# Performance work log

Hardware: AMD Instinct MI355X
Metric: run time of the kernel (lower is better)

Reference implementation:

```python
import jax, jax.numpy as jnp
import numpy as np

MAX_SPAN_WIDTH = 32  # static bound on (end - start) + 1 span length


def setup_inputs() -> dict:
    key = jax.random.key(0)
    k1, k2, k3, k4 = jax.random.split(key, 4)
    B, T, D, N = 4, 2048, 768, 512
    sequence_tensor = jax.random.normal(k1, (B, T, D), dtype=jnp.float32)
    starts = jax.random.randint(k2, (B, N), 0, T - MAX_SPAN_WIDTH)
    widths = jax.random.randint(k3, (B, N), 0, MAX_SPAN_WIDTH)
    span_indices = jnp.stack([starts, starts + widths], axis=-1)  # inclusive ends
    att_w = jax.random.normal(k4, (D, 1), dtype=jnp.float32) * 0.02
    att_b = jnp.zeros((1,), dtype=jnp.float32)
    return {"sequence_tensor": sequence_tensor, "span_indices": span_indices,
            "att_w": att_w, "att_b": att_b}


def reference(sequence_tensor, span_indices, att_w, att_b):
    B, T, D = sequence_tensor.shape
    N = span_indices.shape[1]
    dtype = sequence_tensor.dtype

    # Global attention logits over every token: Linear(D, 1)
    global_logits = (sequence_tensor @ att_w + att_b).squeeze(-1)  # (B, T)

    starts = span_indices[..., 0]
    ends = span_indices[..., 1]           # inclusive
    widths = ends - starts                # (B, N)

    r = jnp.arange(MAX_SPAN_WIDTH)[None, None, :]          # (1, 1, W)
    span_mask = (r <= widths[..., None]).astype(dtype)     # (B, N, W)
    raw_idx = ends[..., None] - r                          # count back from end
    span_mask = span_mask * (raw_idx >= 0).astype(dtype)
    idx = jnp.maximum(raw_idx, 0)                          # (B, N, W), relu of indices

    flat_idx = idx.reshape(B, N * MAX_SPAN_WIDTH)
    # Gather span token embeddings and their attention logits
    span_emb = jnp.take_along_axis(sequence_tensor, flat_idx[..., None], axis=1)
    span_emb = span_emb.reshape(B, N, MAX_SPAN_WIDTH, D)
    span_logits = jnp.take_along_axis(global_logits, flat_idx, axis=1)
    span_logits = span_logits.reshape(B, N, MAX_SPAN_WIDTH)

    # masked_softmax (memory_efficient=False path of the original)
    att = jax.nn.softmax(span_logits * span_mask, axis=-1)
    att = att * span_mask
    att = att / (jnp.sum(att, axis=-1, keepdims=True) + 1e-13)

    # Weighted sum over span positions -> (B, N, D)
    return jnp.einsum("bnw,bnwd->bnd", att, span_emb)
```

## Files before the change

kernel.cpp:

```cpp
#include <hip/hip_runtime.h>

#define SPAN_W 32

__global__ __launch_bounds__(256) void logits_kernel(
    const float* __restrict__ seq,
    const float* __restrict__ att_w,
    const float* __restrict__ att_b,
    float* __restrict__ logits,
    int BT, int D)
{
    int row  = blockIdx.x * 4 + (threadIdx.x >> 6);
    int lane = threadIdx.x & 63;
    if (row >= BT) return;

    const float4* p  = reinterpret_cast<const float4*>(seq + (size_t)row * D);
    const float4* w4 = reinterpret_cast<const float4*>(att_w);
    int d4 = D >> 2;
    float acc = 0.f;
    for (int k = lane; k < d4; k += 64) {
        float4 v = p[k];
        float4 w = w4[k];
        acc += v.x * w.x + v.y * w.y + v.z * w.z + v.w * w.w;
    }
    #pragma unroll
    for (int off = 32; off > 0; off >>= 1)
        acc += __shfl_xor(acc, off);
    if (lane == 0)
        logits[row] = acc + att_b[0];
}

__global__ __launch_bounds__(192) void span_kernel(
    const float* __restrict__ seq,
    const int*   __restrict__ spans,
    const float* __restrict__ logits,
    float*       __restrict__ out,
    int T, int D, int N)
{
    int span = blockIdx.x;
    int b    = span / N;

    int s0 = spans[(size_t)span * 2 + 0];
    int e0 = spans[(size_t)span * 2 + 1];
    int width = e0 - s0;
    (void)s0;

    __shared__ float att[SPAN_W];

    int tid = threadIdx.x;
    if (tid < SPAN_W) {
        int r   = tid;
        int raw = e0 - r;
        bool m  = (r <= width) && (raw >= 0);
        int idx = raw > 0 ? raw : 0;
        float z = m ? logits[(size_t)b * T + idx] : 0.0f;

        float zmax = z;
        #pragma unroll
        for (int off = 16; off > 0; off >>= 1)
            zmax = fmaxf(zmax, __shfl_xor(zmax, off));
        float e = __expf(z - zmax);
        float S = e;
        #pragma unroll
        for (int off = 16; off > 0; off >>= 1)
            S += __shfl_xor(S, off);
        float t = m ? (e / S) : 0.0f;
        float Tt = t;
        #pragma unroll
        for (int off = 16; off > 0; off >>= 1)
            Tt += __shfl_xor(Tt, off);
        att[r] = t / (Tt + 1e-13f);
    }
    __syncthreads();

    int nvalid = width + 1;
    if (nvalid > SPAN_W) nvalid = SPAN_W;
    if (nvalid < 1) nvalid = 1;

    const float* base = seq + (size_t)b * T * D;

    float4 acc = make_float4(0.f, 0.f, 0.f, 0.f);
    for (int w0 = 0; w0 < nvalid; w0 += 8) {
        float4 v[8];
        float  a[8];
        #pragma unroll
        for (int i = 0; i < 8; ++i) {
            int w   = w0 + i;
            int idx = e0 - w; if (idx < 0) idx = 0;
            a[i] = att[w];
            v[i] = reinterpret_cast<const float4*>(base + (size_t)idx * D)[tid];
        }
        #pragma unroll
        for (int i = 0; i < 8; ++i) {
            acc.x += a[i] * v[i].x;
            acc.y += a[i] * v[i].y;
            acc.z += a[i] * v[i].z;
            acc.w += a[i] * v[i].w;
        }
    }
    reinterpret_cast<float4*>(out + (size_t)span * D)[tid] = acc;
}

extern "C" void kernel_launch(void* const* d_in, const int* in_sizes, int n_in,
                              void* d_out, int out_size, void* d_ws, size_t ws_size,
                              hipStream_t stream)
{
    const float* seq   = (const float*)d_in[0];
    const int*   spans = (const int*)  d_in[1];
    const float* att_w = (const float*)d_in[2];
    const float* att_b = (const float*)d_in[3];
    float*       out   = (float*)d_out;
    float*       lg    = (float*)d_ws;

    const int D  = in_sizes[2];
    const int B  = 4;
    const int BT = in_sizes[0] / D;
    const int T  = BT / B;
    const int BN = out_size / D;
    const int N  = BN / B;

    int blocks1 = (BT + 3) / 4;
    logits_kernel<<<blocks1, 256, 0, stream>>>(seq, att_w, att_b, lg, BT, D);
    span_kernel<<<BN, 192, 0, stream>>>(seq, spans, lg, out, T, D, N);
}
```

Before: 90.54 us.

## Fuse logits computation into span kernel, recomputing per-span token logits

Removes the separate pass that computed attention logits for every token and instead has each span block compute dot products only for its own span rows before the softmax. This eliminates one full read of the sequence and a kernel launch. In exchange, logits for tokens in overlapping spans are recomputed, each span's rows are read twice (once for logits, once for the weighted sum), and an extra serialized phase precedes the gather. The logit loop assumes D equals 768 via fixed float4 offsets.

```diff
diff --git a/kernel.cpp b/kernel.cpp
--- a/kernel.cpp
+++ b/kernel.cpp
@@ -2,37 +2,11 @@
 
 #define SPAN_W 32
 
-__global__ __launch_bounds__(256) void logits_kernel(
+__global__ __launch_bounds__(192) void fused_span_kernel(
     const float* __restrict__ seq,
+    const int*   __restrict__ spans,
     const float* __restrict__ att_w,
     const float* __restrict__ att_b,
-    float* __restrict__ logits,
-    int BT, int D)
-{
-    int row  = blockIdx.x * 4 + (threadIdx.x >> 6);
-    int lane = threadIdx.x & 63;
-    if (row >= BT) return;
-
-    const float4* p  = reinterpret_cast<const float4*>(seq + (size_t)row * D);
-    const float4* w4 = reinterpret_cast<const float4*>(att_w);
-    int d4 = D >> 2;
-    float acc = 0.f;
-    for (int k = lane; k < d4; k += 64) {
-        float4 v = p[k];
-        float4 w = w4[k];
-        acc += v.x * w.x + v.y * w.y + v.z * w.z + v.w * w.w;
-    }
-    #pragma unroll
-    for (int off = 32; off > 0; off >>= 1)
-        acc += __shfl_xor(acc, off);
-    if (lane == 0)
-        logits[row] = acc + att_b[0];
-}
-
-__global__ __launch_bounds__(192) void span_kernel(
-    const float* __restrict__ seq,
-    const int*   __restrict__ spans,
-    const float* __restrict__ logits,
     float*       __restrict__ out,
     int T, int D, int N)
 {
@@ -42,18 +16,45 @@
     int s0 = spans[(size_t)span * 2 + 0];
     int e0 = spans[(size_t)span * 2 + 1];
     int width = e0 - s0;
-    (void)s0;
 
+    int tid  = threadIdx.x;
+    int wave = tid >> 6;
+    int lane = tid & 63;
+
+    __shared__ float zbuf[SPAN_W];
     __shared__ float att[SPAN_W];
 
-    int tid = threadIdx.x;
+    const float*  base = seq + (size_t)b * T * D;
+    const float4* w4   = reinterpret_cast<const float4*>(att_w);
+
+    float4 wa = w4[lane];
+    float4 wb = w4[lane + 64];
+    float4 wc = w4[lane + 128];
+    float  bias = att_b[0];
+
+    for (int r = wave; r < SPAN_W; r += 3) {
+        int  raw = e0 - r;
+        bool m   = (r <= width) && (raw >= 0);
+        float z  = 0.f;
+        if (m) {
+            const float4* p =
+                reinterpret_cast<const float4*>(base + (size_t)raw * D);
+            float4 v0 = p[lane], v1 = p[lane + 64], v2 = p[lane + 128];
+            z = v0.x*wa.x + v0.y*wa.y + v0.z*wa.z + v0.w*wa.w
+              + v1.x*wb.x + v1.y*wb.y + v1.z*wb.z + v1.w*wb.w
+              + v2.x*wc.x + v2.y*wc.y + v2.z*wc.z + v2.w*wc.w;
+        }
+        #pragma unroll
+        for (int off = 32; off > 0; off >>= 1)
+            z += __shfl_xor(z, off);
+        if (lane == 0)
+            zbuf[r] = m ? (z + bias) : 0.f;
+    }
+    __syncthreads();
+
     if (tid < SPAN_W) {
         int r   = tid;
-        int raw = e0 - r;
-        bool m  = (r <= width) && (raw >= 0);
-        int idx = raw > 0 ? raw : 0;
-        float z = m ? logits[(size_t)b * T + idx] : 0.0f;
-
+        float z = zbuf[r];
         float zmax = z;
         #pragma unroll
         for (int off = 16; off > 0; off >>= 1)
@@ -63,6 +64,7 @@
         #pragma unroll
         for (int off = 16; off > 0; off >>= 1)
             S += __shfl_xor(S, off);
+        bool  m = (r <= width) && (e0 - r >= 0);
         float t = m ? (e / S) : 0.0f;
         float Tt = t;
         #pragma unroll
@@ -75,8 +77,6 @@
     int nvalid = width + 1;
     if (nvalid > SPAN_W) nvalid = SPAN_W;
     if (nvalid < 1) nvalid = 1;
-
-    const float* base = seq + (size_t)b * T * D;
 
     float4 acc = make_float4(0.f, 0.f, 0.f, 0.f);
     for (int w0 = 0; w0 < nvalid; w0 += 8) {
@@ -109,7 +109,6 @@
     const float* att_w = (const float*)d_in[2];
     const float* att_b = (const float*)d_in[3];
     float*       out   = (float*)d_out;
-    float*       lg    = (float*)d_ws;
 
     const int D  = in_sizes[2];
     const int B  = 4;
@@ -118,7 +117,5 @@
     const int BN = out_size / D;
     const int N  = BN / B;
 
-    int blocks1 = (BT + 3) / 4;
-    logits_kernel<<<blocks1, 256, 0, stream>>>(seq, att_w, att_b, lg, BT, D);
-    span_kernel<<<BN, 192, 0, stream>>>(seq, spans, lg, out, T, D, N);
+    fused_span_kernel<<<BN, 192, 0, stream>>>(seq, spans, att_w, att_b, out, T, D, N);
 }
```

Measured after the change: 99.26 us. 1.1x slower.
